# Optimization experiments

Hardware: AMD Instinct MI355X
Metric: run time of the kernel (lower is better)

Reference implementation:

```python
import jax, jax.numpy as jnp
import numpy as np

N, FEAT, H, D, E, C = 3072, 512, 8, 8, 100000, 2
ALPHA = 0.2  # LeakyReLU slope
NEG_INF = -9e15


def setup_inputs() -> dict:
    key = jax.random.key(0)
    ks = jax.random.split(key, 12)
    x = jax.random.normal(ks[0], (N, FEAT), dtype=jnp.float32)
    adj = (jax.random.uniform(ks[1], (N, N)) < 0.002).astype(jnp.float32)
    adj = jnp.maximum(adj, jnp.eye(N, dtype=jnp.float32))
    L = jax.random.randint(ks[2], (E,), 0, N)
    R = jax.random.randint(ks[3], (E,), 0, N)
    label = jax.random.randint(ks[4], (E,), 0, C)
    s = 1.0 / np.sqrt(FEAT)
    W = jax.random.uniform(ks[5], (H, FEAT, D), minval=-s, maxval=s, dtype=jnp.float32)
    sa = 1.0 / np.sqrt(2 * D)
    a1 = jax.random.uniform(ks[6], (H, D), minval=-sa, maxval=sa, dtype=jnp.float32)
    a2 = jax.random.uniform(ks[7], (H, D), minval=-sa, maxval=sa, dtype=jnp.float32)
    s1 = 1.0 / np.sqrt(H * D * 2)
    W1 = jax.random.uniform(ks[8], (H * D * 2, 64), minval=-s1, maxval=s1, dtype=jnp.float32)
    b1 = jnp.zeros((64,), dtype=jnp.float32)
    s2 = 1.0 / np.sqrt(64)
    W2 = jax.random.uniform(ks[9], (64, C), minval=-s2, maxval=s2, dtype=jnp.float32)
    b2 = jnp.zeros((C,), dtype=jnp.float32)
    return {"x": x, "adj": adj, "L": L, "R": R, "label": label,
            "W": W, "a1": a1, "a2": a2, "W1": W1, "b1": b1, "W2": W2, "b2": b2}


def _encoder(x, adj, W, a1, a2):
    # Wh: [H, N, D]
    Wh = jnp.einsum('nf,hfd->hnd', x, W)
    # broadcast attention logits: e[h,i,j] = leaky_relu(Wh_i.a1 + Wh_j.a2)
    s1 = jnp.einsum('hnd,hd->hn', Wh, a1)[:, :, None]   # [H,N,1]
    s2 = jnp.einsum('hnd,hd->hn', Wh, a2)[:, None, :]   # [H,1,N]
    e = jax.nn.leaky_relu(s1 + s2, negative_slope=ALPHA)  # [H,N,N]
    e = jnp.where(adj[None] > 0, e, NEG_INF)
    att = jax.nn.softmax(e, axis=-1)                      # [H,N,N]
    h = jnp.einsum('hnm,hmd->hnd', att, Wh)               # [H,N,D]
    h = jax.nn.elu(h)                                     # concat=True -> ELU
    # concat heads: [N, H*D]
    return jnp.transpose(h, (1, 0, 2)).reshape(x.shape[0], -1)


def reference(x, adj, L, R, label, W, a1, a2, W1, b1, W2, b2):
    emb = _encoder(x, adj, W, a1, a2)            # [N, 64]
    lr = jnp.concatenate([emb[L], emb[R]], axis=1)  # [E, 128]
    hcls = jax.nn.relu(lr @ W1 + b1)
    logits = hcls @ W2 + b2                       # [E, C]
    logp = jax.nn.log_softmax(logits, axis=-1)
    nll = -jnp.take_along_axis(logp, label[:, None], axis=1)[:, 0]
    return jnp.mean(nll)
```

## Files before the change

### kernel.cpp

```cpp
#include <hip/hip_runtime.h>
#include <math.h>

#define NN 3072
#define FEAT 512
#define HD 64
#define NE 100000
#define ALPHA 0.2f
#define CAP 96
#define CAPP 97
#define AROWS 8
#define WH_BLOCKS 768
#define K5_BLOCKS 2048

__global__ __launch_bounds__(256) void k_stage1(const float* __restrict__ adj, const float* __restrict__ x,
                                                const float* __restrict__ W, const float* __restrict__ a1,
                                                const float* __restrict__ a2, int* __restrict__ nbr,
                                                int* __restrict__ cnt, float* __restrict__ Wh,
                                                float* __restrict__ s1t, float* __restrict__ s2t) {
    __shared__ float xs[4][FEAT];
    __shared__ float part[4][4][HD];
    __shared__ int   wcnt[4];
    int b = blockIdx.x;
    int tid = threadIdx.x;
    int wid = tid >> 6, lane = tid & 63;

    if (b >= WH_BLOCKS) {
        int i = b - WH_BLOCKS;
        const float4* row4 = (const float4*)&adj[(size_t)i * NN];
        float4 v[3];
        #pragma unroll
        for (int c = 0; c < 3; ++c) v[c] = row4[wid * 192 + c * 64 + lane];
        unsigned long long lmask = (1ull << lane) - 1ull;
        int wc = 0;
        unsigned long long masks[12];
        #pragma unroll
        for (int c = 0; c < 3; ++c) {
            #pragma unroll
            for (int k = 0; k < 4; ++k) {
                float vk = k == 0 ? v[c].x : k == 1 ? v[c].y : k == 2 ? v[c].z : v[c].w;
                unsigned long long m = __ballot(vk > 0.f);
                masks[c * 4 + k] = m;
                wc += __popcll(m);
            }
        }
        if (lane == 0) wcnt[wid] = wc;
        __syncthreads();
        int base = 0;
        #pragma unroll
        for (int w2 = 0; w2 < 4; ++w2) if (w2 < wid) base += wcnt[w2];
        #pragma unroll
        for (int c = 0; c < 3; ++c) {
            #pragma unroll
            for (int k = 0; k < 4; ++k) {
                unsigned long long m = masks[c * 4 + k];
                if ((m >> lane) & 1ull) {
                    int pos = base + __popcll(m & lmask);
                    if (pos < CAP) nbr[i * CAP + pos] = wid * 768 + c * 256 + lane * 4 + k;
                }
                base += __popcll(m);
            }
        }
        if (tid == 0) {
            int tot = wcnt[0] + wcnt[1] + wcnt[2] + wcnt[3];
            cnt[i] = tot < CAP ? tot : CAP;
        }
    } else {
        int n0 = b * 4;
        for (int idx = tid; idx < 512; idx += 256) {
            int r = idx >> 7, fq = idx & 127;
            *(float4*)&xs[r][fq * 4] = ((const float4*)x)[(size_t)(n0 + r) * (FEAT / 4) + fq];
        }
        __syncthreads();
        int fsub = lane >> 4, h = (lane >> 1) & 7, dq = lane & 1;
        const float4* W4 = (const float4*)W;
        int base4 = h * 1024 + dq;
        int f0 = wid * (FEAT / 4);
        float4 acc0 = {0.f,0.f,0.f,0.f}, acc1 = acc0, acc2 = acc0, acc3 = acc0;
        #pragma unroll 4
        for (int f4 = 0; f4 < 32; ++f4) {
            int f = f0 + f4 * 4 + fsub;
            float4 w4 = W4[base4 + f * 2];
            float x0 = xs[0][f], x1 = xs[1][f], x2 = xs[2][f], x3 = xs[3][f];
            acc0.x = fmaf(x0, w4.x, acc0.x); acc0.y = fmaf(x0, w4.y, acc0.y);
            acc0.z = fmaf(x0, w4.z, acc0.z); acc0.w = fmaf(x0, w4.w, acc0.w);
            acc1.x = fmaf(x1, w4.x, acc1.x); acc1.y = fmaf(x1, w4.y, acc1.y);
            acc1.z = fmaf(x1, w4.z, acc1.z); acc1.w = fmaf(x1, w4.w, acc1.w);
            acc2.x = fmaf(x2, w4.x, acc2.x); acc2.y = fmaf(x2, w4.y, acc2.y);
            acc2.z = fmaf(x2, w4.z, acc2.z); acc2.w = fmaf(x2, w4.w, acc2.w);
            acc3.x = fmaf(x3, w4.x, acc3.x); acc3.y = fmaf(x3, w4.y, acc3.y);
            acc3.z = fmaf(x3, w4.z, acc3.z); acc3.w = fmaf(x3, w4.w, acc3.w);
        }
        #define RED4(A) \
            A.x += __shfl_xor(A.x, 16, 64); A.x += __shfl_xor(A.x, 32, 64); \
            A.y += __shfl_xor(A.y, 16, 64); A.y += __shfl_xor(A.y, 32, 64); \
            A.z += __shfl_xor(A.z, 16, 64); A.z += __shfl_xor(A.z, 32, 64); \
            A.w += __shfl_xor(A.w, 16, 64); A.w += __shfl_xor(A.w, 32, 64);
        RED4(acc0) RED4(acc1) RED4(acc2) RED4(acc3)
        #undef RED4
        if (fsub == 0) {
            int o = h * 8 + dq * 4;
            *(float4*)&part[wid][0][o] = acc0;
            *(float4*)&part[wid][1][o] = acc1;
            *(float4*)&part[wid][2][o] = acc2;
            *(float4*)&part[wid][3][o] = acc3;
        }
        __syncthreads();
        int n = n0 + wid;
        float v = part[0][wid][lane] + part[1][wid][lane] + part[2][wid][lane] + part[3][wid][lane];
        Wh[n * HD + lane] = v;
        float t1 = v * a1[lane];
        float t2 = v * a2[lane];
        for (int m = 1; m < 8; m <<= 1) {
            t1 += __shfl_xor(t1, m, 64);
            t2 += __shfl_xor(t2, m, 64);
        }
        if ((lane & 7) == 0) {
            int h2 = lane >> 3;
            s1t[n * 8 + h2] = t1;
            s2t[n * 8 + h2] = t2;
        }
    }
}

__global__ __launch_bounds__(512) void k_attn_pq(const float* __restrict__ Wh, const float* __restrict__ s1t,
                                                 const float* __restrict__ s2t, const int* __restrict__ nbr,
                                                 const int* __restrict__ cnt, const float* __restrict__ W1,
                                                 const float* __restrict__ b1, float* __restrict__ P,
                                                 float* __restrict__ Q) {
    __shared__ float W1s[2 * HD][HD];
    __shared__ int   jbuf[AROWS][CAP];
    __shared__ float ebuf[AROWS][8][CAPP];
    __shared__ float es[AROWS][HD];
    int tid = threadIdx.x;
    int wid = tid >> 6;
    int lane = tid & 63;
    int i = blockIdx.x * AROWS + wid;
    int h = lane >> 3, d = lane & 7;
    int ni = cnt[i];
    float s1i = s1t[i * 8 + h];
    for (int k = lane; k < CAP; k += 64)
        if (k < ni) jbuf[wid][k] = nbr[i * CAP + k];
    for (int idx = tid; idx < 2048; idx += 512)
        ((float4*)W1s)[idx] = ((const float4*)W1)[idx];
    __syncthreads();
    float mloc = -INFINITY;
    for (int k = d; k < ni; k += 8) {
        int j = jbuf[wid][k];
        float ev = s1i + s2t[j * 8 + h];
        ev = ev > 0.f ? ev : ALPHA * ev;
        ebuf[wid][h][k] = ev;
        mloc = fmaxf(mloc, ev);
    }
    mloc = fmaxf(mloc, __shfl_xor(mloc, 1, 8));
    mloc = fmaxf(mloc, __shfl_xor(mloc, 2, 8));
    mloc = fmaxf(mloc, __shfl_xor(mloc, 4, 8));
    __syncthreads();
    float denom = 0.f, acc = 0.f;
    for (int k = 0; k < ni; ++k) {
        float p = __expf(ebuf[wid][h][k] - mloc);
        denom += p;
        acc = fmaf(p, Wh[jbuf[wid][k] * HD + lane], acc);
    }
    float o = acc / denom;
    o = o > 0.f ? o : expm1f(o);
    es[wid][lane] = o;
    __syncthreads();
    float p = b1[lane], q = 0.f;
    #pragma unroll 8
    for (int k = 0; k < HD; ++k) {
        float e = es[wid][k];
        p = fmaf(e, W1s[k][lane], p);
        q = fmaf(e, W1s[HD + k][lane], q);
    }
    P[i * HD + lane] = p;
    Q[i * HD + lane] = q;
}

__global__ __launch_bounds__(256) void k_cls(const float* __restrict__ P, const float* __restrict__ Q,
                                             const int* __restrict__ L, const int* __restrict__ R,
                                             const int* __restrict__ label, const float* __restrict__ W2,
                                             const float* __restrict__ b2, float* __restrict__ partials) {
    int tid = threadIdx.x;
    int sl = tid & 15;
    int g = (blockIdx.x * 256 + tid) >> 4;
    float2 wa = *(const float2*)&W2[(sl * 4 + 0) * 2];
    float2 wb = *(const float2*)&W2[(sl * 4 + 1) * 2];
    float2 wc = *(const float2*)&W2[(sl * 4 + 2) * 2];
    float2 wd = *(const float2*)&W2[(sl * 4 + 3) * 2];
    float b20 = b2[0], b21 = b2[1];

    int e0 = g, e1 = g + 32768, e2 = g + 65536;
    int ln0 = L[e0], rn0 = R[e0], lb0 = label[e0];
    int ln1 = L[e1], rn1 = R[e1], lb1 = label[e1];
    int ln2 = L[e2], rn2 = R[e2], lb2 = label[e2];
    float4 p0 = *(const float4*)&P[ln0 * HD + sl * 4];
    float4 q0 = *(const float4*)&Q[rn0 * HD + sl * 4];
    float4 p1 = *(const float4*)&P[ln1 * HD + sl * 4];
    float4 q1 = *(const float4*)&Q[rn1 * HD + sl * 4];
    float4 p2 = *(const float4*)&P[ln2 * HD + sl * 4];
    float4 q2 = *(const float4*)&Q[rn2 * HD + sl * 4];

    float v00 = fmaxf(p0.x + q0.x, 0.f), v01 = fmaxf(p0.y + q0.y, 0.f);
    float v02 = fmaxf(p0.z + q0.z, 0.f), v03 = fmaxf(p0.w + q0.w, 0.f);
    float v10 = fmaxf(p1.x + q1.x, 0.f), v11 = fmaxf(p1.y + q1.y, 0.f);
    float v12 = fmaxf(p1.z + q1.z, 0.f), v13 = fmaxf(p1.w + q1.w, 0.f);
    float v20 = fmaxf(p2.x + q2.x, 0.f), v21 = fmaxf(p2.y + q2.y, 0.f);
    float v22 = fmaxf(p2.z + q2.z, 0.f), v23 = fmaxf(p2.w + q2.w, 0.f);

    float t00 = v00 * wa.x + v01 * wb.x + v02 * wc.x + v03 * wd.x;
    float t01 = v00 * wa.y + v01 * wb.y + v02 * wc.y + v03 * wd.y;
    float t10 = v10 * wa.x + v11 * wb.x + v12 * wc.x + v13 * wd.x;
    float t11 = v10 * wa.y + v11 * wb.y + v12 * wc.y + v13 * wd.y;
    float t20 = v20 * wa.x + v21 * wb.x + v22 * wc.x + v23 * wd.x;
    float t21 = v20 * wa.y + v21 * wb.y + v22 * wc.y + v23 * wd.y;
    #pragma unroll
    for (int m = 1; m < 16; m <<= 1) {
        t00 += __shfl_xor(t00, m, 64);  t01 += __shfl_xor(t01, m, 64);
        t10 += __shfl_xor(t10, m, 64);  t11 += __shfl_xor(t11, m, 64);
        t20 += __shfl_xor(t20, m, 64);  t21 += __shfl_xor(t21, m, 64);
    }
    float sum;
    {
        float l0 = t00 + b20, l1 = t01 + b21;
        float mx = fmaxf(l0, l1);
        sum = mx + __logf(__expf(l0 - mx) + __expf(l1 - mx)) - (lb0 ? l1 : l0);
        l0 = t10 + b20; l1 = t11 + b21; mx = fmaxf(l0, l1);
        sum += mx + __logf(__expf(l0 - mx) + __expf(l1 - mx)) - (lb1 ? l1 : l0);
        l0 = t20 + b20; l1 = t21 + b21; mx = fmaxf(l0, l1);
        sum += mx + __logf(__expf(l0 - mx) + __expf(l1 - mx)) - (lb2 ? l1 : l0);
    }
    if (g + 98304 < NE) {
        int e3 = g + 98304;
        int ln3 = L[e3], rn3 = R[e3], lb3 = label[e3];
        float4 p3 = *(const float4*)&P[ln3 * HD + sl * 4];
        float4 q3 = *(const float4*)&Q[rn3 * HD + sl * 4];
        float w0 = fmaxf(p3.x + q3.x, 0.f), w1 = fmaxf(p3.y + q3.y, 0.f);
        float w2 = fmaxf(p3.z + q3.z, 0.f), w3 = fmaxf(p3.w + q3.w, 0.f);
        float t30 = w0 * wa.x + w1 * wb.x + w2 * wc.x + w3 * wd.x;
        float t31 = w0 * wa.y + w1 * wb.y + w2 * wc.y + w3 * wd.y;
        #pragma unroll
        for (int m = 1; m < 16; m <<= 1) {
            t30 += __shfl_xor(t30, m, 64);  t31 += __shfl_xor(t31, m, 64);
        }
        float l0 = t30 + b20, l1 = t31 + b21;
        float mx = fmaxf(l0, l1);
        sum += mx + __logf(__expf(l0 - mx) + __expf(l1 - mx)) - (lb3 ? l1 : l0);
    }
    sum = (sl == 0) ? sum : 0.f;
    #pragma unroll
    for (int m = 1; m < 64; m <<= 1) sum += __shfl_xor(sum, m, 64);
    __shared__ float wsum[4];
    if ((tid & 63) == 0) wsum[tid >> 6] = sum;
    __syncthreads();
    if (tid == 0) partials[blockIdx.x] = wsum[0] + wsum[1] + wsum[2] + wsum[3];
}

__global__ __launch_bounds__(1024) void k_reduce(const float* __restrict__ partials, float* __restrict__ out) {
    __shared__ float sh[1024];
    int t = threadIdx.x;
    sh[t] = partials[t] + partials[t + 1024];
    __syncthreads();
    for (int s = 512; s > 0; s >>= 1) {
        if (t < s) sh[t] += sh[t + s];
        __syncthreads();
    }
    if (t == 0) out[0] = sh[0] / (float)NE;
}

extern "C" void kernel_launch(void* const* d_in, const int* in_sizes, int n_in,
                              void* d_out, int out_size, void* d_ws, size_t ws_size,
                              hipStream_t stream) {
    const float* x     = (const float*)d_in[0];
    const float* adj   = (const float*)d_in[1];
    const int*   L     = (const int*)d_in[2];
    const int*   R     = (const int*)d_in[3];
    const int*   label = (const int*)d_in[4];
    const float* W     = (const float*)d_in[5];
    const float* a1    = (const float*)d_in[6];
    const float* a2    = (const float*)d_in[7];
    const float* W1    = (const float*)d_in[8];
    const float* b1    = (const float*)d_in[9];
    const float* W2    = (const float*)d_in[10];
    const float* b2    = (const float*)d_in[11];

    char* ws = (char*)d_ws;
    float* Wh       = (float*)(ws + 0);
    float* s1t      = (float*)(ws + 786432);
    float* s2t      = (float*)(ws + 884736);
    int*   cnt      = (int*)  (ws + 983040);
    int*   nbr      = (int*)  (ws + 995328);
    float* P        = (float*)(ws + 2174976);
    float* Q        = (float*)(ws + 2961408);
    float* partials = (float*)(ws + 3747840);

    k_stage1<<<WH_BLOCKS + NN, 256, 0, stream>>>(adj, x, W, a1, a2, nbr, cnt, Wh, s1t, s2t);
    k_attn_pq<<<NN / AROWS, 512, 0, stream>>>(Wh, s1t, s2t, nbr, cnt, W1, b1, P, Q);
    k_cls<<<K5_BLOCKS, 256, 0, stream>>>(P, Q, L, R, label, W2, b2, partials);
    k_reduce<<<1, 1024, 0, stream>>>(partials, (float*)d_out);
}
```

Measured before the change: 34.55 us.

## Widen stage1 blocks to 8 nodes and 2 adj rows, unroll attention gather

Stage1 blocks grow to 512 threads. The Wh projection now computes 8 nodes per block, so each W load is reused across twice as many rows with 8 accumulators per lane. Adjacency-compaction blocks now handle two rows each, which halves the block count. The attention aggregation loop is unrolled by two with separate accumulators to expose more independent Wh gathers; in exchange the kernel uses more registers and has fewer blocks in flight.

```diff
diff --git a/kernel.cpp b/kernel.cpp
--- a/kernel.cpp
+++ b/kernel.cpp
@@ -9,27 +9,29 @@
 #define CAP 96
 #define CAPP 97
 #define AROWS 8
-#define WH_BLOCKS 768
+#define WH_BLOCKS 384
 #define K5_BLOCKS 2048
 
-__global__ __launch_bounds__(256) void k_stage1(const float* __restrict__ adj, const float* __restrict__ x,
+__global__ __launch_bounds__(512) void k_stage1(const float* __restrict__ adj, const float* __restrict__ x,
                                                 const float* __restrict__ W, const float* __restrict__ a1,
                                                 const float* __restrict__ a2, int* __restrict__ nbr,
                                                 int* __restrict__ cnt, float* __restrict__ Wh,
                                                 float* __restrict__ s1t, float* __restrict__ s2t) {
-    __shared__ float xs[4][FEAT];
-    __shared__ float part[4][4][HD];
-    __shared__ int   wcnt[4];
+    __shared__ float xs[8][FEAT];
+    __shared__ float part[8][8][HD];
+    __shared__ int   wcnt[2][4];
     int b = blockIdx.x;
     int tid = threadIdx.x;
     int wid = tid >> 6, lane = tid & 63;
 
     if (b >= WH_BLOCKS) {
-        int i = b - WH_BLOCKS;
+        int sub = wid >> 2;
+        int w4i = wid & 3;
+        int i = (b - WH_BLOCKS) * 2 + sub;
         const float4* row4 = (const float4*)&adj[(size_t)i * NN];
         float4 v[3];
         #pragma unroll
-        for (int c = 0; c < 3; ++c) v[c] = row4[wid * 192 + c * 64 + lane];
+        for (int c = 0; c < 3; ++c) v[c] = row4[w4i * 192 + c * 64 + lane];
         unsigned long long lmask = (1ull << lane) - 1ull;
         int wc = 0;
         unsigned long long masks[12];
@@ -43,11 +45,11 @@
                 wc += __popcll(m);
             }
         }
-        if (lane == 0) wcnt[wid] = wc;
+        if (lane == 0) wcnt[sub][w4i] = wc;
         __syncthreads();
         int base = 0;
         #pragma unroll
-        for (int w2 = 0; w2 < 4; ++w2) if (w2 < wid) base += wcnt[w2];
+        for (int w2 = 0; w2 < 4; ++w2) if (w2 < w4i) base += wcnt[sub][w2];
         #pragma unroll
         for (int c = 0; c < 3; ++c) {
             #pragma unroll
@@ -55,18 +57,20 @@
                 unsigned long long m = masks[c * 4 + k];
                 if ((m >> lane) & 1ull) {
                     int pos = base + __popcll(m & lmask);
-                    if (pos < CAP) nbr[i * CAP + pos] = wid * 768 + c * 256 + lane * 4 + k;
+                    if (pos < CAP) nbr[i * CAP + pos] = w4i * 768 + c * 256 + lane * 4 + k;
                 }
                 base += __popcll(m);
             }
         }
-        if (tid == 0) {
-            int tot = wcnt[0] + wcnt[1] + wcnt[2] + wcnt[3];
+        if (w4i == 0 && lane == 0) {
+            int tot = wcnt[sub][0] + wcnt[sub][1] + wcnt[sub][2] + wcnt[sub][3];
             cnt[i] = tot < CAP ? tot : CAP;
         }
     } else {
-        int n0 = b * 4;
-        for (int idx = tid; idx < 512; idx += 256) {
+        int n0 = b * 8;
+        #pragma unroll
+        for (int t = 0; t < 2; ++t) {
+            int idx = tid + t * 512;
             int r = idx >> 7, fq = idx & 127;
             *(float4*)&xs[r][fq * 4] = ((const float4*)x)[(size_t)(n0 + r) * (FEAT / 4) + fq];
         }
@@ -74,39 +78,54 @@
         int fsub = lane >> 4, h = (lane >> 1) & 7, dq = lane & 1;
         const float4* W4 = (const float4*)W;
         int base4 = h * 1024 + dq;
-        int f0 = wid * (FEAT / 4);
-        float4 acc0 = {0.f,0.f,0.f,0.f}, acc1 = acc0, acc2 = acc0, acc3 = acc0;
+        int f0 = wid * (FEAT / 8);
+        float4 a0 = {0,0,0,0}, a1v = a0, a2v = a0, a3 = a0, a4 = a0, a5 = a0, a6 = a0, a7 = a0;
         #pragma unroll 4
-        for (int f4 = 0; f4 < 32; ++f4) {
+        for (int f4 = 0; f4 < 16; ++f4) {
             int f = f0 + f4 * 4 + fsub;
             float4 w4 = W4[base4 + f * 2];
             float x0 = xs[0][f], x1 = xs[1][f], x2 = xs[2][f], x3 = xs[3][f];
-            acc0.x = fmaf(x0, w4.x, acc0.x); acc0.y = fmaf(x0, w4.y, acc0.y);
-            acc0.z = fmaf(x0, w4.z, acc0.z); acc0.w = fmaf(x0, w4.w, acc0.w);
-            acc1.x = fmaf(x1, w4.x, acc1.x); acc1.y = fmaf(x1, w4.y, acc1.y);
-            acc1.z = fmaf(x1, w4.z, acc1.z); acc1.w = fmaf(x1, w4.w, acc1.w);
-            acc2.x = fmaf(x2, w4.x, acc2.x); acc2.y = fmaf(x2, w4.y, acc2.y);
-            acc2.z = fmaf(x2, w4.z, acc2.z); acc2.w = fmaf(x2, w4.w, acc2.w);
-            acc3.x = fmaf(x3, w4.x, acc3.x); acc3.y = fmaf(x3, w4.y, acc3.y);
-            acc3.z = fmaf(x3, w4.z, acc3.z); acc3.w = fmaf(x3, w4.w, acc3.w);
+            float x4 = xs[4][f], x5 = xs[5][f], x6 = xs[6][f], x7 = xs[7][f];
+            a0.x = fmaf(x0, w4.x, a0.x); a0.y = fmaf(x0, w4.y, a0.y);
+            a0.z = fmaf(x0, w4.z, a0.z); a0.w = fmaf(x0, w4.w, a0.w);
+            a1v.x = fmaf(x1, w4.x, a1v.x); a1v.y = fmaf(x1, w4.y, a1v.y);
+            a1v.z = fmaf(x1, w4.z, a1v.z); a1v.w = fmaf(x1, w4.w, a1v.w);
+            a2v.x = fmaf(x2, w4.x, a2v.x); a2v.y = fmaf(x2, w4.y, a2v.y);
+            a2v.z = fmaf(x2, w4.z, a2v.z); a2v.w = fmaf(x2, w4.w, a2v.w);
+            a3.x = fmaf(x3, w4.x, a3.x); a3.y = fmaf(x3, w4.y, a3.y);
+            a3.z = fmaf(x3, w4.z, a3.z); a3.w = fmaf(x3, w4.w, a3.w);
+            a4.x = fmaf(x4, w4.x, a4.x); a4.y = fmaf(x4, w4.y, a4.y);
+            a4.z = fmaf(x4, w4.z, a4.z); a4.w = fmaf(x4, w4.w, a4.w);
+            a5.x = fmaf(x5, w4.x, a5.x); a5.y = fmaf(x5, w4.y, a5.y);
+            a5.z = fmaf(x5, w4.z, a5.z); a5.w = fmaf(x5, w4.w, a5.w);
+            a6.x = fmaf(x6, w4.x, a6.x); a6.y = fmaf(x6, w4.y, a6.y);
+            a6.z = fmaf(x6, w4.z, a6.z); a6.w = fmaf(x6, w4.w, a6.w);
+            a7.x = fmaf(x7, w4.x, a7.x); a7.y = fmaf(x7, w4.y, a7.y);
+            a7.z = fmaf(x7, w4.z, a7.z); a7.w = fmaf(x7, w4.w, a7.w);
         }
         #define RED4(A) \
             A.x += __shfl_xor(A.x, 16, 64); A.x += __shfl_xor(A.x, 32, 64); \
             A.y += __shfl_xor(A.y, 16, 64); A.y += __shfl_xor(A.y, 32, 64); \
             A.z += __shfl_xor(A.z, 16, 64); A.z += __shfl_xor(A.z, 32, 64); \
             A.w += __shfl_xor(A.w, 16, 64); A.w += __shfl_xor(A.w, 32, 64);
-        RED4(acc0) RED4(acc1) RED4(acc2) RED4(acc3)
+        RED4(a0) RED4(a1v) RED4(a2v) RED4(a3) RED4(a4) RED4(a5) RED4(a6) RED4(a7)
         #undef RED4
         if (fsub == 0) {
             int o = h * 8 + dq * 4;
-            *(float4*)&part[wid][0][o] = acc0;
-            *(float4*)&part[wid][1][o] = acc1;
-            *(float4*)&part[wid][2][o] = acc2;
-            *(float4*)&part[wid][3][o] = acc3;
+            *(float4*)&part[wid][0][o] = a0;
+            *(float4*)&part[wid][1][o] = a1v;
+            *(float4*)&part[wid][2][o] = a2v;
+            *(float4*)&part[wid][3][o] = a3;
+            *(float4*)&part[wid][4][o] = a4;
+            *(float4*)&part[wid][5][o] = a5;
+            *(float4*)&part[wid][6][o] = a6;
+            *(float4*)&part[wid][7][o] = a7;
         }
         __syncthreads();
         int n = n0 + wid;
-        float v = part[0][wid][lane] + part[1][wid][lane] + part[2][wid][lane] + part[3][wid][lane];
+        float v = 0.f;
+        #pragma unroll
+        for (int w2 = 0; w2 < 8; ++w2) v += part[w2][wid][lane];
         Wh[n * HD + lane] = v;
         float t1 = v * a1[lane];
         float t2 = v * a2[lane];
@@ -155,22 +174,32 @@
     mloc = fmaxf(mloc, __shfl_xor(mloc, 2, 8));
     mloc = fmaxf(mloc, __shfl_xor(mloc, 4, 8));
     __syncthreads();
-    float denom = 0.f, acc = 0.f;
-    for (int k = 0; k < ni; ++k) {
-        float p = __expf(ebuf[wid][h][k] - mloc);
-        denom += p;
-        acc = fmaf(p, Wh[jbuf[wid][k] * HD + lane], acc);
-    }
-    float o = acc / denom;
+    float den0 = 0.f, den1 = 0.f, ac0 = 0.f, ac1 = 0.f;
+    int k = 0;
+    for (; k + 1 < ni; k += 2) {
+        int j0 = jbuf[wid][k], j1 = jbuf[wid][k + 1];
+        float p0 = __expf(ebuf[wid][h][k] - mloc);
+        float p1 = __expf(ebuf[wid][h][k + 1] - mloc);
+        float w0 = Wh[j0 * HD + lane], w1 = Wh[j1 * HD + lane];
+        den0 += p0; den1 += p1;
+        ac0 = fmaf(p0, w0, ac0);
+        ac1 = fmaf(p1, w1, ac1);
+    }
+    if (k < ni) {
+        float p0 = __expf(ebuf[wid][h][k] - mloc);
+        den0 += p0;
+        ac0 = fmaf(p0, Wh[jbuf[wid][k] * HD + lane], ac0);
+    }
+    float o = (ac0 + ac1) / (den0 + den1);
     o = o > 0.f ? o : expm1f(o);
     es[wid][lane] = o;
     __syncthreads();
     float p = b1[lane], q = 0.f;
     #pragma unroll 8
-    for (int k = 0; k < HD; ++k) {
-        float e = es[wid][k];
-        p = fmaf(e, W1s[k][lane], p);
-        q = fmaf(e, W1s[HD + k][lane], q);
+    for (int kk = 0; kk < HD; ++kk) {
+        float e = es[wid][kk];
+        p = fmaf(e, W1s[kk][lane], p);
+        q = fmaf(e, W1s[HD + kk][lane], q);
     }
     P[i * HD + lane] = p;
     Q[i * HD + lane] = q;
@@ -293,7 +322,7 @@
     float* Q        = (float*)(ws + 2961408);
     float* partials = (float*)(ws + 3747840);
 
-    k_stage1<<<WH_BLOCKS + NN, 256, 0, stream>>>(adj, x, W, a1, a2, nbr, cnt, Wh, s1t, s2t);
+    k_stage1<<<WH_BLOCKS + NN / 2, 512, 0, stream>>>(adj, x, W, a1, a2, nbr, cnt, Wh, s1t, s2t);
     k_attn_pq<<<NN / AROWS, 512, 0, stream>>>(Wh, s1t, s2t, nbr, cnt, W1, b1, P, Q);
     k_cls<<<K5_BLOCKS, 256, 0, stream>>>(P, Q, L, R, label, W2, b2, partials);
     k_reduce<<<1, 1024, 0, stream>>>(partials, (float*)d_out);
```

After: 34.86 us. About the same (+0.9%).

## Replace final reduce kernel with atomicAdd and halve rows per Wh block

Applied to the files above, without the earlier changes.

The separate single-block reduction kernel is removed. k_cls now atomically adds its scaled per-block partial sums straight into the output, which k_stage1 zeroes first, saving one kernel launch and the partials round trip. The Wh projection part of k_stage1 now handles two nodes per block instead of four, doubling its block count for more parallelism at the cost of reading W twice as often. Float atomics make the summation order nondeterministic, and the zeroing relies on stream ordering between kernels.

```diff
diff --git a/kernel.cpp b/kernel.cpp
--- a/kernel.cpp
+++ b/kernel.cpp
@@ -9,23 +9,25 @@
 #define CAP 96
 #define CAPP 97
 #define AROWS 8
-#define WH_BLOCKS 768
+#define WHB2 1536
 #define K5_BLOCKS 2048
 
 __global__ __launch_bounds__(256) void k_stage1(const float* __restrict__ adj, const float* __restrict__ x,
                                                 const float* __restrict__ W, const float* __restrict__ a1,
                                                 const float* __restrict__ a2, int* __restrict__ nbr,
                                                 int* __restrict__ cnt, float* __restrict__ Wh,
-                                                float* __restrict__ s1t, float* __restrict__ s2t) {
-    __shared__ float xs[4][FEAT];
-    __shared__ float part[4][4][HD];
+                                                float* __restrict__ s1t, float* __restrict__ s2t,
+                                                float* __restrict__ out) {
+    __shared__ float xs[2][FEAT];
+    __shared__ float part[4][2][HD];
     __shared__ int   wcnt[4];
     int b = blockIdx.x;
     int tid = threadIdx.x;
     int wid = tid >> 6, lane = tid & 63;
-
-    if (b >= WH_BLOCKS) {
-        int i = b - WH_BLOCKS;
+    if (b == 0 && tid == 0) out[0] = 0.f;
+
+    if (b >= WHB2) {
+        int i = b - WHB2;
         const float4* row4 = (const float4*)&adj[(size_t)i * NN];
         float4 v[3];
         #pragma unroll
@@ -65,8 +67,10 @@
             cnt[i] = tot < CAP ? tot : CAP;
         }
     } else {
-        int n0 = b * 4;
-        for (int idx = tid; idx < 512; idx += 256) {
+        int n0 = b * 2;
+        for (int idx = tid; idx < 256; idx += 256) {}
+        {
+            int idx = tid;
             int r = idx >> 7, fq = idx & 127;
             *(float4*)&xs[r][fq * 4] = ((const float4*)x)[(size_t)(n0 + r) * (FEAT / 4) + fq];
         }
@@ -75,49 +79,46 @@
         const float4* W4 = (const float4*)W;
         int base4 = h * 1024 + dq;
         int f0 = wid * (FEAT / 4);
-        float4 acc0 = {0.f,0.f,0.f,0.f}, acc1 = acc0, acc2 = acc0, acc3 = acc0;
+        float4 acc0 = {0.f,0.f,0.f,0.f}, acc1 = acc0;
         #pragma unroll 4
         for (int f4 = 0; f4 < 32; ++f4) {
             int f = f0 + f4 * 4 + fsub;
             float4 w4 = W4[base4 + f * 2];
-            float x0 = xs[0][f], x1 = xs[1][f], x2 = xs[2][f], x3 = xs[3][f];
+            float x0 = xs[0][f], x1 = xs[1][f];
             acc0.x = fmaf(x0, w4.x, acc0.x); acc0.y = fmaf(x0, w4.y, acc0.y);
             acc0.z = fmaf(x0, w4.z, acc0.z); acc0.w = fmaf(x0, w4.w, acc0.w);
             acc1.x = fmaf(x1, w4.x, acc1.x); acc1.y = fmaf(x1, w4.y, acc1.y);
             acc1.z = fmaf(x1, w4.z, acc1.z); acc1.w = fmaf(x1, w4.w, acc1.w);
-            acc2.x = fmaf(x2, w4.x, acc2.x); acc2.y = fmaf(x2, w4.y, acc2.y);
-            acc2.z = fmaf(x2, w4.z, acc2.z); acc2.w = fmaf(x2, w4.w, acc2.w);
-            acc3.x = fmaf(x3, w4.x, acc3.x); acc3.y = fmaf(x3, w4.y, acc3.y);
-            acc3.z = fmaf(x3, w4.z, acc3.z); acc3.w = fmaf(x3, w4.w, acc3.w);
         }
         #define RED4(A) \
             A.x += __shfl_xor(A.x, 16, 64); A.x += __shfl_xor(A.x, 32, 64); \
             A.y += __shfl_xor(A.y, 16, 64); A.y += __shfl_xor(A.y, 32, 64); \
             A.z += __shfl_xor(A.z, 16, 64); A.z += __shfl_xor(A.z, 32, 64); \
             A.w += __shfl_xor(A.w, 16, 64); A.w += __shfl_xor(A.w, 32, 64);
-        RED4(acc0) RED4(acc1) RED4(acc2) RED4(acc3)
+        RED4(acc0) RED4(acc1)
         #undef RED4
         if (fsub == 0) {
             int o = h * 8 + dq * 4;
             *(float4*)&part[wid][0][o] = acc0;
             *(float4*)&part[wid][1][o] = acc1;
-            *(float4*)&part[wid][2][o] = acc2;
-            *(float4*)&part[wid][3][o] = acc3;
         }
         __syncthreads();
-        int n = n0 + wid;
-        float v = part[0][wid][lane] + part[1][wid][lane] + part[2][wid][lane] + part[3][wid][lane];
-        Wh[n * HD + lane] = v;
-        float t1 = v * a1[lane];
-        float t2 = v * a2[lane];
-        for (int m = 1; m < 8; m <<= 1) {
-            t1 += __shfl_xor(t1, m, 64);
-            t2 += __shfl_xor(t2, m, 64);
-        }
-        if ((lane & 7) == 0) {
-            int h2 = lane >> 3;
-            s1t[n * 8 + h2] = t1;
-            s2t[n * 8 + h2] = t2;
+        if (wid < 2) {
+            int n = n0 + wid;
+            float v = part[0][wid][lane] + part[1][wid][lane]
+                    + part[2][wid][lane] + part[3][wid][lane];
+            Wh[n * HD + lane] = v;
+            float t1 = v * a1[lane];
+            float t2 = v * a2[lane];
+            for (int m = 1; m < 8; m <<= 1) {
+                t1 += __shfl_xor(t1, m, 64);
+                t2 += __shfl_xor(t2, m, 64);
+            }
+            if ((lane & 7) == 0) {
+                int h2 = lane >> 3;
+                s1t[n * 8 + h2] = t1;
+                s2t[n * 8 + h2] = t2;
+            }
         }
     }
 }
@@ -179,7 +180,7 @@
 __global__ __launch_bounds__(256) void k_cls(const float* __restrict__ P, const float* __restrict__ Q,
                                              const int* __restrict__ L, const int* __restrict__ R,
                                              const int* __restrict__ label, const float* __restrict__ W2,
-                                             const float* __restrict__ b2, float* __restrict__ partials) {
+                                             const float* __restrict__ b2, float* __restrict__ out) {
     int tid = threadIdx.x;
     int sl = tid & 15;
     int g = (blockIdx.x * 256 + tid) >> 4;
@@ -252,19 +253,8 @@
     __shared__ float wsum[4];
     if ((tid & 63) == 0) wsum[tid >> 6] = sum;
     __syncthreads();
-    if (tid == 0) partials[blockIdx.x] = wsum[0] + wsum[1] + wsum[2] + wsum[3];
-}
-
-__global__ __launch_bounds__(1024) void k_reduce(const float* __restrict__ partials, float* __restrict__ out) {
-    __shared__ float sh[1024];
-    int t = threadIdx.x;
-    sh[t] = partials[t] + partials[t + 1024];
-    __syncthreads();
-    for (int s = 512; s > 0; s >>= 1) {
-        if (t < s) sh[t] += sh[t + s];
-        __syncthreads();
-    }
-    if (t == 0) out[0] = sh[0] / (float)NE;
+    if (tid == 0)
+        atomicAdd(out, (wsum[0] + wsum[1] + wsum[2] + wsum[3]) * (1.f / (float)NE));
 }
 
 extern "C" void kernel_launch(void* const* d_in, const int* in_sizes, int n_in,
@@ -291,10 +281,9 @@
     int*   nbr      = (int*)  (ws + 995328);
     float* P        = (float*)(ws + 2174976);
     float* Q        = (float*)(ws + 2961408);
-    float* partials = (float*)(ws + 3747840);
-
-    k_stage1<<<WH_BLOCKS + NN, 256, 0, stream>>>(adj, x, W, a1, a2, nbr, cnt, Wh, s1t, s2t);
+    float* outp     = (float*)d_out;
+
+    k_stage1<<<WHB2 + NN, 256, 0, stream>>>(adj, x, W, a1, a2, nbr, cnt, Wh, s1t, s2t, outp);
     k_attn_pq<<<NN / AROWS, 512, 0, stream>>>(Wh, s1t, s2t, nbr, cnt, W1, b1, P, Q);
-    k_cls<<<K5_BLOCKS, 256, 0, stream>>>(P, Q, L, R, label, W2, b2, partials);
-    k_reduce<<<1, 1024, 0, stream>>>(partials, (float*)d_out);
-}
+    k_cls<<<K5_BLOCKS, 256, 0, stream>>>(P, Q, L, R, label, W2, b2, outp);
+}
```

After: 60.50 us. +75.1%, slower.
